# Kernel optimization log

Measured on AMD Instinct MI355X. Metric: run time of the kernel, lower is better.

## Reference

```python
import jax, jax.numpy as jnp
import numpy as np

KS = 3
PAD = 1
N = KS * KS  # 9 sampling points per output pixel


def setup_inputs() -> dict:
    key = jax.random.key(0)
    k1, k2, k3 = jax.random.split(key, 3)
    b, c_in, c_out, h, w = 8, 64, 64, 64, 64
    x = jax.random.normal(k1, (b, c_in, h, w), jnp.float32)
    offset = jax.random.normal(k2, (b, 2 * N, h, w), jnp.float32)
    # learned conv kernel: Conv2d(inc, outc, ks, stride=ks, bias=None)
    weight = jax.random.normal(k3, (c_out, c_in, KS, KS), jnp.float32) * 0.05
    return {"x": x, "offset": offset, "weight": weight}


def _deform_conv(x, offset, weight):
    b, c, h, w = x.shape
    # reorder interleaved offsets (x0,y0,x1,y1,...) -> (x0..xN-1, y0..yN-1)
    offset = jnp.concatenate([offset[:, 0::2], offset[:, 1::2]], axis=1)
    # zero padding
    xp = jnp.pad(x, ((0, 0), (0, 0), (PAD, PAD), (PAD, PAD)))
    Hp, Wp = h + 2 * PAD, w + 2 * PAD
    dt = offset.dtype
    # p_n: kernel-relative offsets, (1, 2N, 1, 1)
    r = jnp.arange(-(KS - 1) // 2, (KS - 1) // 2 + 1, dtype=dt)
    pnx, pny = jnp.meshgrid(r, r, indexing="ij")
    p_n = jnp.concatenate([pnx.ravel(), pny.ravel()]).reshape(1, 2 * N, 1, 1)
    # p_0: base sampling grid in padded coords (starts at 1), (1, 2N, h, w)
    gx, gy = jnp.meshgrid(jnp.arange(1, h + 1, dtype=dt), jnp.arange(1, w + 1, dtype=dt), indexing="ij")
    p_0 = jnp.concatenate([jnp.broadcast_to(gx, (1, N, h, w)), jnp.broadcast_to(gy, (1, N, h, w))], axis=1)
    p = (p_0 + p_n + offset).transpose(0, 2, 3, 1)  # (b, h, w, 2N)

    fp = jnp.floor(p)
    q_lt_x = jnp.clip(fp[..., :N], 0, Hp - 1)
    q_lt_y = jnp.clip(fp[..., N:], 0, Wp - 1)
    q_rb_x = jnp.clip(fp[..., :N] + 1, 0, Hp - 1)
    q_rb_y = jnp.clip(fp[..., N:] + 1, 0, Wp - 1)

    # snap out-of-range sampling points to floor (as in the torch code)
    mask_x = (p[..., :N] < PAD) | (p[..., :N] > Hp - 1 - PAD)
    mask_y = (p[..., N:] < PAD) | (p[..., N:] > Wp - 1 - PAD)
    mask = jnp.concatenate([mask_x, mask_y], axis=-1)
    p = jnp.where(mask, fp, p)
    px = jnp.clip(p[..., :N], 0, Hp - 1)
    py = jnp.clip(p[..., N:], 0, Wp - 1)

    # bilinear weights
    g_lt = (1 + (q_lt_x - px)) * (1 + (q_lt_y - py))
    g_rb = (1 - (q_rb_x - px)) * (1 - (q_rb_y - py))
    g_lb = (1 + (q_lt_x - px)) * (1 - (q_rb_y - py))
    g_rt = (1 - (q_rb_x - px)) * (1 + (q_lt_y - py))

    xf = xp.reshape(b, c, Hp * Wp)

    def gather(qx, qy):
        idx = (qx * Wp + qy).astype(jnp.int32).reshape(b, -1)  # (b, h*w*N)
        out = jax.vmap(lambda xf_b, i_b: xf_b[:, i_b])(xf, idx)  # (b, c, h*w*N)
        return out.reshape(b, c, h, w, N)

    x_lt = gather(q_lt_x, q_lt_y)
    x_rb = gather(q_rb_x, q_rb_y)
    x_lb = gather(q_lt_x, q_rb_y)
    x_rt = gather(q_rb_x, q_lt_y)

    xo = (g_lt[:, None] * x_lt + g_rb[:, None] * x_rb
          + g_lb[:, None] * x_lb + g_rt[:, None] * x_rt)  # (b, c, h, w, N)
    # rearrange N = ks*ks sampling points into a (h*ks, w*ks) spatial grid
    xo = xo.reshape(b, c, h, w, KS, KS).transpose(0, 1, 2, 4, 3, 5).reshape(b, c, h * KS, w * KS)
    # conv with kernel ks, stride ks, no bias
    out = jax.lax.conv_general_dilated(
        xo, weight, window_strides=(KS, KS), padding="VALID",
        dimension_numbers=("NCHW", "OIHW", "NCHW"))
    return out


def reference(x, offset, weight):
    return _deform_conv(x, offset, weight)
```

## Files before the change

kernel.cpp:

```cpp
#include <hip/hip_runtime.h>
#include <hip/hip_bf16.h>
#include <hip/hip_fp16.h>

#define N9 9
#define TPX 32
#define CIN 64
#define COUT 64
#define HH 64
#define WW 64
#define BB 8
#define KTOT 576
#define SROW 584
#define NTASK (N9 * TPX)

typedef short bf16x8 __attribute__((ext_vector_type(8)));
typedef float f32x4 __attribute__((ext_vector_type(4)));
typedef unsigned int uint32x4 __attribute__((ext_vector_type(4)));

__global__ __launch_bounds__(256) void prep_fused(const float* __restrict__ x,
                                                  const float* __restrict__ w,
                                                  ushort* __restrict__ xt,
                                                  short* __restrict__ wt) {
    __shared__ float tile[64][65];
    const int t = threadIdx.x;
    if (blockIdx.x >= BB * HH) {
        int idx = (blockIdx.x - BB * HH) * 256 + t;
        if (idx < COUT * KTOT) {
            int co = idx / KTOT;
            int r  = idx - co * KTOT;
            int ci = r / N9;
            int n  = r - ci * N9;
            __hip_bfloat16 h = __float2bfloat16(w[idx]);
            wt[co * KTOT + n * CIN + ci] = *reinterpret_cast<short*>(&h);
        }
        return;
    }
    const int bh = blockIdx.x;
    const int b = bh >> 6, h = bh & 63;
    const int r0 = t >> 6;
    const int c  = t & 63;
    const float* xp = x + ((b * CIN) * HH + h) * WW;
    #pragma unroll
    for (int s = 0; s < 16; ++s) {
        const int ci = s * 4 + r0;
        tile[ci][c] = xp[ci * (HH * WW) + c];
    }
    __syncthreads();
    ushort* xo = xt + (b * HH + h) * (WW * CIN);
    #pragma unroll
    for (int s = 0; s < 16; ++s) {
        const int w2 = s * 4 + r0;
        __hip_bfloat16 hv = __float2bfloat16(tile[c][w2]);
        xo[w2 * CIN + c] = *reinterpret_cast<ushort*>(&hv);
    }
}

__device__ __forceinline__ void blend4(const uint32x4 u, const float gc, float* f) {
    #pragma unroll
    for (int p = 0; p < 4; ++p) {
        union { unsigned int i; float v; } lo, hi;
        lo.i = u[p] << 16;
        hi.i = u[p] & 0xffff0000u;
        f[2 * p]     += gc * lo.v;
        f[2 * p + 1] += gc * hi.v;
    }
}

__global__ __launch_bounds__(256, 4) void deform_main(
    const ushort* __restrict__ xt,
    const float* __restrict__ off,
    const short* __restrict__ wtb,
    float* __restrict__ out) {

    __shared__ unsigned int s_g01[NTASK];
    __shared__ unsigned int s_g23[NTASK];
    __shared__ int          s_bse[NTASK];
    __attribute__((aligned(16))) __shared__ short S[TPX][SROW];

    const int t    = threadIdx.x;
    const int lane = t & 63;
    const int wave = t >> 6;

    const int logical = (blockIdx.x & 7) * 128 + (blockIdx.x >> 3);
    const int pix0 = logical * TPX;
    const int b    = pix0 >> 12;
    const int i    = (pix0 >> 6) & 63;
    const int j0   = pix0 & 63;

    const int lr = lane & 15;
    const int kq = lane >> 4;
    const short* arow = wtb + (wave * 16 + lr) * KTOT + kq * 8;
    bf16x8 afr[18];
    #pragma unroll
    for (int kk = 0; kk < 18; ++kk)
        afr[kk] = *reinterpret_cast<const bf16x8*>(arow + kk * 32);

    for (int task = t; task < NTASK; task += 256) {
        const int n  = task >> 5;
        const int px = task & 31;
        const int j  = j0 + px;
        const float offx = off[(((b * 18) + 2 * n) * HH + i) * WW + j];
        const float offy = off[(((b * 18) + 2 * n + 1) * HH + i) * WW + j];
        const float pxf = (float)(i + n / 3) + offx;
        const float pyf = (float)(j + n % 3) + offy;
        const float fpx = floorf(pxf);
        const float fpy = floorf(pyf);
        const float qltx = fminf(fmaxf(fpx, 0.f), 65.f);
        const float qlty = fminf(fmaxf(fpy, 0.f), 65.f);
        const float qrbx = fminf(fmaxf(fpx + 1.f, 0.f), 65.f);
        const float qrby = fminf(fmaxf(fpy + 1.f, 0.f), 65.f);
        const bool mx = (pxf < 1.f) || (pxf > 64.f);
        const bool my = (pyf < 1.f) || (pyf > 64.f);
        const float Px = fminf(fmaxf(mx ? fpx : pxf, 0.f), 65.f);
        const float Py = fminf(fmaxf(my ? fpy : pyf, 0.f), 65.f);
        float ul = 1.f + (qltx - Px);
        float ur = 1.f - (qrbx - Px);
        float wl = 1.f + (qlty - Py);
        float wr = 1.f - (qrby - Py);
        const int ltx = (int)qltx, lty = (int)qlty;
        const int rbx = (int)qrbx, rby = (int)qrby;
        if (ltx < 1 || ltx > 64) ul = 0.f;
        if (rbx < 1 || rbx > 64) ur = 0.f;
        if (lty < 1 || lty > 64) wl = 0.f;
        if (rby < 1 || rby > 64) wr = 0.f;
        const int r = ltx - 1, c = lty - 1;
        const int rp = min(max(r, 0), 62), cp = min(max(c, 0), 62);
        const float u0 = (rp == r ? ul : 0.f) + (rp == rbx - 1 ? ur : 0.f);
        const float u1 = (rp + 1 == r ? ul : 0.f) + (rp + 1 == rbx - 1 ? ur : 0.f);
        const float w0 = (cp == c ? wl : 0.f) + (cp == rby - 1 ? wr : 0.f);
        const float w1 = (cp + 1 == c ? wl : 0.f) + (cp + 1 == rby - 1 ? wr : 0.f);
        __half2 h01 = __floats2half2_rn(u0 * w0, u0 * w1);
        __half2 h23 = __floats2half2_rn(u1 * w0, u1 * w1);
        s_g01[task] = *reinterpret_cast<unsigned int*>(&h01);
        s_g23[task] = *reinterpret_cast<unsigned int*>(&h23);
        s_bse[task] = (rp * WW + cp) * CIN;
    }
    __syncthreads();

    const ushort* xb = xt + b * (HH * WW * CIN);
    #pragma unroll 3
    for (int it = 0; it < 9; ++it) {
        const int slot = it * 256 + t;
        const int task = slot >> 3;
        const int g8   = slot & 7;
        const int bse  = s_bse[task] + g8 * 8;
        const float2 g01 = __half22float2(*reinterpret_cast<const __half2*>(&s_g01[task]));
        const float2 g23 = __half22float2(*reinterpret_cast<const __half2*>(&s_g23[task]));
        const uint32x4 u00 = *(const uint32x4*)(xb + bse);
        const uint32x4 u01 = *(const uint32x4*)(xb + bse + CIN);
        const uint32x4 u10 = *(const uint32x4*)(xb + bse + WW * CIN);
        const uint32x4 u11 = *(const uint32x4*)(xb + bse + WW * CIN + CIN);
        float f[8] = {0.f, 0.f, 0.f, 0.f, 0.f, 0.f, 0.f, 0.f};
        blend4(u00, g01.x, f);
        blend4(u01, g01.y, f);
        blend4(u10, g23.x, f);
        blend4(u11, g23.y, f);
        bf16x8 sv;
        #pragma unroll
        for (int jj = 0; jj < 8; ++jj) {
            __hip_bfloat16 h = __float2bfloat16(f[jj]);
            sv[jj] = *reinterpret_cast<short*>(&h);
        }
        const int px = task & 31;
        const int n  = task >> 5;
        *reinterpret_cast<bf16x8*>(&S[px][n * CIN + g8 * 8]) = sv;
    }
    __syncthreads();

    f32x4 acc0 = {0.f, 0.f, 0.f, 0.f};
    f32x4 acc1 = {0.f, 0.f, 0.f, 0.f};
    const short* b0 = &S[lr][kq * 8];
    const short* b1 = &S[lr + 16][kq * 8];
    #pragma unroll
    for (int kk = 0; kk < 18; ++kk) {
        bf16x8 bf0 = *reinterpret_cast<const bf16x8*>(b0 + kk * 32);
        bf16x8 bf1 = *reinterpret_cast<const bf16x8*>(b1 + kk * 32);
        acc0 = __builtin_amdgcn_mfma_f32_16x16x32_bf16(afr[kk], bf0, acc0, 0, 0, 0);
        acc1 = __builtin_amdgcn_mfma_f32_16x16x32_bf16(afr[kk], bf1, acc1, 0, 0, 0);
    }
    #pragma unroll
    for (int v = 0; v < 4; ++v) {
        const int co = wave * 16 + kq * 4 + v;
        float* op = out + ((b * COUT + co) * HH + i) * WW + j0;
        op[lr]      = acc0[v];
        op[16 + lr] = acc1[v];
    }
}

extern "C" void kernel_launch(void* const* d_in, const int* in_sizes, int n_in,
                              void* d_out, int out_size, void* d_ws, size_t ws_size,
                              hipStream_t stream) {
    const float* x   = (const float*)d_in[0];
    const float* off = (const float*)d_in[1];
    const float* w   = (const float*)d_in[2];
    float* out = (float*)d_out;
    short* wtb  = (short*)d_ws;
    ushort* xt  = (ushort*)((char*)d_ws + 131072);

    const int prep_blocks = BB * HH + (COUT * KTOT + 255) / 256;
    hipLaunchKernelGGL(prep_fused, dim3(prep_blocks), dim3(256), 0, stream,
                       x, w, xt, wtb);
    hipLaunchKernelGGL(deform_main, dim3(BB * HH * WW / TPX), dim3(256), 0, stream,
                       xt, off, wtb, out);
}
```

Baseline: 28.18 us.

## Pipeline bilinear gather with MFMA in three stages and stream weight fragments

```diff
diff --git a/kernel.cpp b/kernel.cpp
--- a/kernel.cpp
+++ b/kernel.cpp
@@ -15,7 +15,12 @@
 
 typedef short bf16x8 __attribute__((ext_vector_type(8)));
 typedef float f32x4 __attribute__((ext_vector_type(4)));
+typedef float f32x2 __attribute__((ext_vector_type(2)));
 typedef unsigned int uint32x4 __attribute__((ext_vector_type(4)));
+
+__device__ __forceinline__ float uasf(unsigned int u) {
+    union { unsigned int i; float f; } c; c.i = u; return c.f;
+}
 
 __global__ __launch_bounds__(256) void prep_fused(const float* __restrict__ x,
                                                   const float* __restrict__ w,
@@ -55,17 +60,6 @@
     }
 }
 
-__device__ __forceinline__ void blend4(const uint32x4 u, const float gc, float* f) {
-    #pragma unroll
-    for (int p = 0; p < 4; ++p) {
-        union { unsigned int i; float v; } lo, hi;
-        lo.i = u[p] << 16;
-        hi.i = u[p] & 0xffff0000u;
-        f[2 * p]     += gc * lo.v;
-        f[2 * p + 1] += gc * hi.v;
-    }
-}
-
 __global__ __launch_bounds__(256, 4) void deform_main(
     const ushort* __restrict__ xt,
     const float* __restrict__ off,
@@ -80,6 +74,8 @@
     const int t    = threadIdx.x;
     const int lane = t & 63;
     const int wave = t >> 6;
+    const int g8   = t & 7;
+    const int t8   = t >> 3;
 
     const int logical = (blockIdx.x & 7) * 128 + (blockIdx.x >> 3);
     const int pix0 = logical * TPX;
@@ -90,10 +86,7 @@
     const int lr = lane & 15;
     const int kq = lane >> 4;
     const short* arow = wtb + (wave * 16 + lr) * KTOT + kq * 8;
-    bf16x8 afr[18];
-    #pragma unroll
-    for (int kk = 0; kk < 18; ++kk)
-        afr[kk] = *reinterpret_cast<const bf16x8*>(arow + kk * 32);
+    const ushort* xb = xt + b * (HH * WW * CIN);
 
     for (int task = t; task < NTASK; task += 256) {
         const int n  = task >> 5;
@@ -135,49 +128,101 @@
         s_g23[task] = *reinterpret_cast<unsigned int*>(&h23);
         s_bse[task] = (rp * WW + cp) * CIN;
     }
-    __syncthreads();
-
-    const ushort* xb = xt + b * (HH * WW * CIN);
-    #pragma unroll 3
-    for (int it = 0; it < 9; ++it) {
-        const int slot = it * 256 + t;
-        const int task = slot >> 3;
-        const int g8   = slot & 7;
-        const int bse  = s_bse[task] + g8 * 8;
-        const float2 g01 = __half22float2(*reinterpret_cast<const __half2*>(&s_g01[task]));
-        const float2 g23 = __half22float2(*reinterpret_cast<const __half2*>(&s_g23[task]));
-        const uint32x4 u00 = *(const uint32x4*)(xb + bse);
-        const uint32x4 u01 = *(const uint32x4*)(xb + bse + CIN);
-        const uint32x4 u10 = *(const uint32x4*)(xb + bse + WW * CIN);
-        const uint32x4 u11 = *(const uint32x4*)(xb + bse + WW * CIN + CIN);
-        float f[8] = {0.f, 0.f, 0.f, 0.f, 0.f, 0.f, 0.f, 0.f};
-        blend4(u00, g01.x, f);
-        blend4(u01, g01.y, f);
-        blend4(u10, g23.x, f);
-        blend4(u11, g23.y, f);
-        bf16x8 sv;
-        #pragma unroll
-        for (int jj = 0; jj < 8; ++jj) {
-            __hip_bfloat16 h = __float2bfloat16(f[jj]);
-            sv[jj] = *reinterpret_cast<short*>(&h);
-        }
-        const int px = task & 31;
-        const int n  = task >> 5;
-        *reinterpret_cast<bf16x8*>(&S[px][n * CIN + g8 * 8]) = sv;
-    }
-    __syncthreads();
 
     f32x4 acc0 = {0.f, 0.f, 0.f, 0.f};
     f32x4 acc1 = {0.f, 0.f, 0.f, 0.f};
-    const short* b0 = &S[lr][kq * 8];
-    const short* b1 = &S[lr + 16][kq * 8];
-    #pragma unroll
-    for (int kk = 0; kk < 18; ++kk) {
-        bf16x8 bf0 = *reinterpret_cast<const bf16x8*>(b0 + kk * 32);
-        bf16x8 bf1 = *reinterpret_cast<const bf16x8*>(b1 + kk * 32);
-        acc0 = __builtin_amdgcn_mfma_f32_16x16x32_bf16(afr[kk], bf0, acc0, 0, 0, 0);
-        acc1 = __builtin_amdgcn_mfma_f32_16x16x32_bf16(afr[kk], bf1, acc1, 0, 0, 0);
-    }
+
+    #define GLOADS(G, u)                                                      \
+        _Pragma("unroll")                                                     \
+        for (int it = 0; it < 3; ++it) {                                      \
+            const int task = 96 * (G) + 32 * it + t8;                         \
+            const int bse  = s_bse[task] + g8 * 8;                            \
+            u[0][it] = *(const uint32x4*)(xb + bse);                          \
+            u[1][it] = *(const uint32x4*)(xb + bse + CIN);                    \
+            u[2][it] = *(const uint32x4*)(xb + bse + WW * CIN);               \
+            u[3][it] = *(const uint32x4*)(xb + bse + WW * CIN + CIN);         \
+        }
+
+    #define GBLEND(G, u)                                                      \
+        _Pragma("unroll")                                                     \
+        for (int it = 0; it < 3; ++it) {                                      \
+            const int task = 96 * (G) + 32 * it + t8;                         \
+            const float2 g01 = __half22float2(*reinterpret_cast<const __half2*>(&s_g01[task])); \
+            const float2 g23 = __half22float2(*reinterpret_cast<const __half2*>(&s_g23[task])); \
+            f32x2 f0 = {0.f, 0.f}, f1 = {0.f, 0.f}, f2 = {0.f, 0.f}, f3 = {0.f, 0.f}; \
+            _Pragma("unroll")                                                 \
+            for (int cc = 0; cc < 4; ++cc) {                                  \
+                const uint32x4 uv = u[cc][it];                                \
+                const float gc = (cc == 0) ? g01.x : (cc == 1) ? g01.y : (cc == 2) ? g23.x : g23.y; \
+                f0 += gc * (f32x2){uasf(uv[0] << 16), uasf(uv[0] & 0xffff0000u)}; \
+                f1 += gc * (f32x2){uasf(uv[1] << 16), uasf(uv[1] & 0xffff0000u)}; \
+                f2 += gc * (f32x2){uasf(uv[2] << 16), uasf(uv[2] & 0xffff0000u)}; \
+                f3 += gc * (f32x2){uasf(uv[3] << 16), uasf(uv[3] & 0xffff0000u)}; \
+            }                                                                 \
+            bf16x8 sv;                                                        \
+            { __hip_bfloat16 h;                                               \
+              h = __float2bfloat16(f0.x); sv[0] = *reinterpret_cast<short*>(&h); \
+              h = __float2bfloat16(f0.y); sv[1] = *reinterpret_cast<short*>(&h); \
+              h = __float2bfloat16(f1.x); sv[2] = *reinterpret_cast<short*>(&h); \
+              h = __float2bfloat16(f1.y); sv[3] = *reinterpret_cast<short*>(&h); \
+              h = __float2bfloat16(f2.x); sv[4] = *reinterpret_cast<short*>(&h); \
+              h = __float2bfloat16(f2.y); sv[5] = *reinterpret_cast<short*>(&h); \
+              h = __float2bfloat16(f3.x); sv[6] = *reinterpret_cast<short*>(&h); \
+              h = __float2bfloat16(f3.y); sv[7] = *reinterpret_cast<short*>(&h); } \
+            const int px = task & 31;                                         \
+            const int n  = task >> 5;                                         \
+            *reinterpret_cast<bf16x8*>(&S[px][n * CIN + g8 * 8]) = sv;        \
+        }
+
+    #define LOADAF(G, af)                                                     \
+        _Pragma("unroll")                                                     \
+        for (int k6 = 0; k6 < 6; ++k6)                                        \
+            af[k6] = *reinterpret_cast<const bf16x8*>(arow + ((G) * 6 + k6) * 32);
+
+    #define MFMAR(G, af)                                                      \
+        _Pragma("unroll")                                                     \
+        for (int k6 = 0; k6 < 6; ++k6) {                                      \
+            bf16x8 b0 = *reinterpret_cast<const bf16x8*>(&S[lr][((G) * 6 + k6) * 32 + kq * 8]);      \
+            bf16x8 b1 = *reinterpret_cast<const bf16x8*>(&S[lr + 16][((G) * 6 + k6) * 32 + kq * 8]); \
+            acc0 = __builtin_amdgcn_mfma_f32_16x16x32_bf16(af[k6], b0, acc0, 0, 0, 0); \
+            acc1 = __builtin_amdgcn_mfma_f32_16x16x32_bf16(af[k6], b1, acc1, 0, 0, 0); \
+        }
+
+    __syncthreads();
+
+    {
+        uint32x4 u[4][3];
+        GLOADS(0, u)
+        GBLEND(0, u)
+    }
+    __syncthreads();
+
+    {
+        bf16x8 af[6];
+        LOADAF(0, af)
+        uint32x4 u[4][3];
+        GLOADS(1, u)
+        MFMAR(0, af)
+        GBLEND(1, u)
+    }
+    __syncthreads();
+
+    {
+        bf16x8 af[6];
+        LOADAF(1, af)
+        uint32x4 u[4][3];
+        GLOADS(2, u)
+        MFMAR(1, af)
+        GBLEND(2, u)
+    }
+    __syncthreads();
+
+    {
+        bf16x8 af[6];
+        LOADAF(2, af)
+        MFMAR(2, af)
+    }
+
     #pragma unroll
     for (int v = 0; v < 4; ++v) {
         const int co = wave * 16 + kq * 4 + v;
```

After: 26.13 us. 1.08x faster.
